# Kernel optimization log

Hardware: AMD Instinct MI355X
Metric: run time of the kernel (lower is better)

Reference implementation:

```python
import jax, jax.numpy as jnp
import numpy as np

B, C, T, H = 256, 8, 1024, 512
WB_INC = 0.05  # task_data_generator.wb_inc


def setup_inputs() -> dict:
    key = jax.random.key(0)
    ks = jax.random.split(key, 8)
    # arms/time strictly positive to keep the likelihood division well-conditioned
    inputs = jax.random.uniform(ks[0], (B, C, T), dtype=jnp.float32) + 0.5
    w_in = jax.random.normal(ks[1], (H, 6), dtype=jnp.float32) / np.sqrt(6.0).astype(np.float32)
    b_in = jax.random.normal(ks[2], (H,), dtype=jnp.float32) * 0.01
    w_rec = jax.random.normal(ks[3], (H, H), dtype=jnp.float32) / np.sqrt(float(H)).astype(np.float32)
    b_rec = jax.random.normal(ks[4], (H,), dtype=jnp.float32) * 0.01
    w_key = jax.random.normal(ks[5], (2, H), dtype=jnp.float32) / np.sqrt(float(H)).astype(np.float32)
    b_key = jax.random.normal(ks[6], (2,), dtype=jnp.float32) * 0.01
    # pre-drawn standard normals for the data-dependent noise injection (one per batch per step)
    z = jax.random.normal(ks[7], (T - 1, B), dtype=jnp.float32)
    return {"inputs": inputs, "w_in": w_in, "b_in": b_in, "w_rec": w_rec,
            "b_rec": b_rec, "w_key": w_key, "b_key": b_key, "z": z}


def _likelihood(tm, arms):
    # ((tm - arm) / (0.15*arm))^2, zeroed where tm == 0
    prs = ((tm[:, None] - arms) / (0.15 * arms)) ** 2
    return jnp.where(tm[:, None] == 0.0, 0.0, prs)


def _forward(inputs, w_in, b_in, w_rec, b_rec, w_key, b_key, z):
    Bsz, _, Tn = inputs.shape
    Hn = w_rec.shape[0]
    in_arms = inputs[:, :6, :]
    tm1 = inputs[:, 6, :]  # (B, T), never modified
    tm2 = inputs[:, 7, :]  # (B, T), receives cumulative noise offsets
    idx_tm1 = jnp.argmax(tm1, axis=1)          # (B,)
    ts = jnp.arange(1, Tn)
    tm1_done = ts[:, None] > idx_tm1[None, :]  # (T-1, B)
    arms_pri = jnp.moveaxis(in_arms[:, :2, 1:], 2, 0)  # (T-1, B, 2)
    arms_sec = jnp.moveaxis(in_arms[:, 2:, 1:], 2, 0)  # (T-1, B, 4)
    tm1_seq = tm1[:, 1:].T                              # (T-1, B)
    tm2_seq = tm2[:, 1:].T                              # (T-1, B)

    def step(carry, xs):
        h_pre, key_h_pre, side_h_pre, offset = carry
        ap, asec, t1, t2o, done, zt = xs
        side_h = key_h_pre > 0.5
        arms_sum = asec[:, :2] * key_h_pre[:, None] + asec[:, 2:] * (1.0 - key_h_pre)[:, None]
        closer1 = jnp.argmin(jnp.abs(ap - t1[:, None]), axis=1) == 0
        away = side_h != closer1
        switched = (side_h != side_h_pre) & done & away
        # in-place suffix update in_time[b,1,t:] += N(0, |wb_inc*tm2_t|) == cumulative per-batch offset
        t2_cur = t2o + offset
        offset = offset + jnp.where(switched, zt * jnp.abs(WB_INC * t2_cur), 0.0)
        t2_eff = t2o + offset
        pr1 = _likelihood(t1, ap)
        pr2 = _likelihood(t2_eff, arms_sum)
        prs_t = jnp.concatenate([pr1, pr2], axis=1)          # (B, 4)
        inp_t = jnp.concatenate([ap, arms_sum, t1[:, None], t2_eff[:, None]], axis=1)  # (B, 6)
        h_t = jnp.tanh(inp_t @ w_in.T + b_in + h_pre @ w_rec.T + b_rec)
        key_t = jax.nn.sigmoid(h_t @ w_key.T + b_key)        # (B, 2)
        return (h_t, key_t[:, 0], side_h, offset), (h_t, prs_t, key_t, t2_eff)

    carry0 = (jnp.zeros((Bsz, Hn), dtype=inputs.dtype),
              jnp.ones((Bsz,), dtype=inputs.dtype),
              jnp.ones((Bsz,), dtype=bool),
              jnp.zeros((Bsz,), dtype=inputs.dtype))
    _, (hs_s, prs_s, keys_s, tm2_s) = jax.lax.scan(
        step, carry0, (arms_pri, arms_sec, tm1_seq, tm2_seq, tm1_done, z))
    # loop starts at t=1; t=0 slots stay zero
    hs = jnp.concatenate([jnp.zeros((Bsz, Hn, 1), dtype=inputs.dtype), jnp.moveaxis(hs_s, 0, 2)], axis=2)
    prs = jnp.concatenate([jnp.zeros((Bsz, 4, 1), dtype=inputs.dtype), jnp.moveaxis(prs_s, 0, 2)], axis=2)
    keys = jnp.concatenate([jnp.zeros((Bsz, 2, 1), dtype=inputs.dtype), jnp.moveaxis(keys_s, 0, 2)], axis=2)
    tm2_mod = jnp.concatenate([tm2[:, :1], tm2_s.T], axis=1)
    tm_modified = jnp.stack([tm1, tm2_mod], axis=1)  # (B, 2, T)
    return keys, prs, hs, tm_modified


def reference(inputs, w_in, b_in, w_rec, b_rec, w_key, b_key, z):
    return _forward(inputs, w_in, b_in, w_rec, b_rec, w_key, b_key, z)
```

## Files before the change

kernel.cpp:

```cpp
#include <hip/hip_runtime.h>
#include <math.h>

#define TN 1024
#define HH 512
#define BB 256
#define NTHR 512
#define NW48 48
#define TSTRIDE 136

#define OFF_KEYS 0L
#define OFF_PRS  524288L
#define OFF_HS   1572864L
#define OFF_TM   135790592L

typedef float f32x4 __attribute__((ext_vector_type(4)));
typedef _Float16 f16x2 __attribute__((ext_vector_type(2)));

__device__ __forceinline__ float sigm(float x) { return 1.0f / (1.0f + expf(-x)); }

__device__ __forceinline__ float dot2(unsigned a, unsigned b, float c) {
#if __has_builtin(__builtin_amdgcn_fdot2)
    return __builtin_amdgcn_fdot2(__builtin_bit_cast(f16x2, a),
                                  __builtin_bit_cast(f16x2, b), c, false);
#else
    const f16x2 x = __builtin_bit_cast(f16x2, a);
    const f16x2 y = __builtin_bit_cast(f16x2, b);
    return fmaf((float)x.y, (float)y.y, fmaf((float)x.x, (float)y.x, c));
#endif
}

__global__ __launch_bounds__(256) void conv_fp16(const float* __restrict__ w,
                                                 _Float16* __restrict__ o) {
    const int i = (blockIdx.x * 256 + threadIdx.x) * 4;
    const f32x4 v = *(const f32x4*)(w + i);
    _Float16 r[4];
    #pragma unroll
    for (int k = 0; k < 4; ++k) r[k] = (_Float16)v[k];
    *(unsigned long long*)(o + i) = *(const unsigned long long*)r;
}

__global__ __launch_bounds__(NTHR, 2)
__attribute__((amdgpu_waves_per_eu(2, 2)))
void rnn_fused(
    const float* __restrict__ in, const float* __restrict__ w_in,
    const float* __restrict__ b_in, const float* __restrict__ b_rec,
    const float* __restrict__ w_key, const float* __restrict__ b_key,
    const float* __restrict__ z, float* __restrict__ out,
    const _Float16* __restrict__ whf)
{
    __shared__ __align__(16) _Float16 wtail[HH][TSTRIDE];
    __shared__ __align__(16) float tbuf[HH][9];
    __shared__ __align__(16) _Float16 hsh[2][HH];
    __shared__ float keysT[2][2][16];
    __shared__ float prsT[2][4][16];
    __shared__ float tmT[2][16];
    __shared__ float inp6[8];
    __shared__ float kred[8][2];

    const int tid = threadIdx.x;
    const int bb  = blockIdx.x;
    const int wv  = tid >> 6, ln = tid & 63;
    const float* inb = in + (long)bb * 8 * TN;
    const unsigned* wrow = (const unsigned*)(whf + (long)tid * HH);

    unsigned wreg[NW48 * 4];
    #pragma unroll
    for (int i = 0; i < NW48; ++i) {
        const uint4 v = *(const uint4*)(wrow + i * 4);
        wreg[i * 4 + 0] = v.x; wreg[i * 4 + 1] = v.y;
        wreg[i * 4 + 2] = v.z; wreg[i * 4 + 3] = v.w;
    }
    #pragma unroll
    for (int i = 0; i < NW48 * 4; ++i) asm volatile("" : "+v"(wreg[i]));

    {
        const uint4* src = (const uint4*)(wrow + 192);
        #pragma unroll
        for (int i = 0; i < 16; ++i) *(uint4*)&wtail[tid][i * 8] = src[i];
    }

    const float bs  = b_in[tid] + b_rec[tid];
    const float wk0 = w_key[tid], wk1 = w_key[HH + tid];
    const float* wip = w_in + tid * 6;
    const float wi0 = wip[0], wi1 = wip[1], wi2 = wip[2];
    const float wi3 = wip[3], wi4 = wip[4], wi5 = wip[5];

    hsh[0][tid] = (_Float16)0.0f;
    tbuf[tid][0] = 0.0f;
    if (tid < 256) {
        f32x4 v = *(const f32x4*)(inb + 6 * TN + tid * 4);
        __builtin_nontemporal_store(v, (f32x4*)(out + OFF_TM + (long)bb * 2 * TN + tid * 4));
    }
    if (tid == 0) {
        keysT[0][0][0] = 0.f; keysT[0][1][0] = 0.f;
        prsT[0][0][0] = 0.f; prsT[0][1][0] = 0.f;
        prsT[0][2][0] = 0.f; prsT[0][3][0] = 0.f;
        tmT[0][0] = inb[7 * TN];
    }
    int idxm = 0;
    if (wv == 0) {
        const float* tp = inb + 6 * TN;
        float bv = -3.0e38f; int bi = 0;
        for (int i = 0; i < 16; ++i) { int tt = i * 64 + ln; float v = tp[tt]; if (v > bv) { bv = v; bi = tt; } }
        #pragma unroll
        for (int m = 1; m < 64; m <<= 1) {
            float ov = __shfl_xor(bv, m); int oi = __shfl_xor(bi, m);
            if (ov > bv || (ov == bv && oi < bi)) { bv = ov; bi = oi; }
        }
        idxm = bi;
    }
    float kh = 1.0f, off = 0.0f; int side_pre = 1;
    float q0=0,q1=0,q2=0,q3=0,q4=0,q5=0,q6=0,q7=0,qz=0;
    const float bk0 = b_key[0], bk1 = b_key[1];
    if (tid == 0) {
        q0=inb[1]; q1=inb[TN+1]; q2=inb[2*TN+1]; q3=inb[3*TN+1];
        q4=inb[4*TN+1]; q5=inb[5*TN+1]; q6=inb[6*TN+1]; q7=inb[7*TN+1];
        qz=z[bb];
    }
    __syncthreads();

    for (int t = 1; t < TN; ++t) {
        const int par1 = (t - 1) & 1, par2 = t & 1;
        const int tile = (t >> 4) & 1, sl = t & 15;

        if (tid == 0) {
            if (t > 1) {
                float k0 = 0.f, k1 = 0.f;
                #pragma unroll
                for (int w = 0; w < 8; ++w) { k0 += kred[w][0]; k1 += kred[w][1]; }
                const float key0 = sigm(k0 + bk0), key1 = sigm(k1 + bk1);
                const int pt = t - 1;
                keysT[(pt >> 4) & 1][0][pt & 15] = key0;
                keysT[(pt >> 4) & 1][1][pt & 15] = key1;
                kh = key0;
            }
            const int side = (kh > 0.5f);
            const float as0 = q2 * kh + q4 * (1.0f - kh);
            const float as1 = q3 * kh + q5 * (1.0f - kh);
            const int closer1 = (fabsf(q0 - q6) <= fabsf(q1 - q6));
            const int done = (t > idxm);
            const int sw = ((side != side_pre) && done && (side != closer1));
            const float t2c = q7 + off;
            if (sw) off += qz * fabsf(0.05f * t2c);
            const float t2e = q7 + off;
            side_pre = side;
            float u0 = (q6 - q0) / (0.15f * q0);    float pr10 = (q6 == 0.f) ? 0.f : u0 * u0;
            float u1 = (q6 - q1) / (0.15f * q1);    float pr11 = (q6 == 0.f) ? 0.f : u1 * u1;
            float u2 = (t2e - as0) / (0.15f * as0); float pr20 = (t2e == 0.f) ? 0.f : u2 * u2;
            float u3 = (t2e - as1) / (0.15f * as1); float pr21 = (t2e == 0.f) ? 0.f : u3 * u3;
            prsT[tile][0][sl] = pr10; prsT[tile][1][sl] = pr11;
            prsT[tile][2][sl] = pr20; prsT[tile][3][sl] = pr21;
            tmT[tile][sl] = t2e;
            inp6[0] = q0; inp6[1] = q1; inp6[2] = as0;
            inp6[3] = as1; inp6[4] = q6; inp6[5] = t2e;
            const int tn = (t < TN - 1) ? t + 1 : t;
            q0 = inb[tn]; q1 = inb[TN + tn]; q2 = inb[2 * TN + tn]; q3 = inb[3 * TN + tn];
            q4 = inb[4 * TN + tn]; q5 = inb[5 * TN + tn]; q6 = inb[6 * TN + tn]; q7 = inb[7 * TN + tn];
            qz = z[(long)(tn - 1) * BB + bb];
        }

        float a0 = 0.f, a1 = 0.f, a2 = 0.f, a3 = 0.f;
        const unsigned* hb = (const unsigned*)&hsh[par1][0];
        #pragma unroll
        for (int i = 0; i < NW48; ++i) {
            const uint4 hu = *(const uint4*)(hb + i * 4);
            a0 = dot2(wreg[i * 4 + 0], hu.x, a0);
            a1 = dot2(wreg[i * 4 + 1], hu.y, a1);
            a2 = dot2(wreg[i * 4 + 2], hu.z, a2);
            a3 = dot2(wreg[i * 4 + 3], hu.w, a3);
        }
        #pragma unroll
        for (int i = 0; i < 16; ++i) {
            const uint4 hu = *(const uint4*)(hb + 192 + i * 4);
            const uint4 wu = *(const uint4*)&wtail[tid][i * 8];
            a0 = dot2(wu.x, hu.x, a0);
            a1 = dot2(wu.y, hu.y, a1);
            a2 = dot2(wu.z, hu.z, a2);
            a3 = dot2(wu.w, hu.w, a3);
        }
        const float sdot = (a0 + a1) + (a2 + a3);
        __syncthreads();

        {
            const float s = sdot + bs
                          + wi0 * inp6[0] + wi1 * inp6[1] + wi2 * inp6[2]
                          + wi3 * inp6[3] + wi4 * inp6[4] + wi5 * inp6[5];
            const float h = tanhf(s);
            hsh[par2][tid] = (_Float16)h;
            tbuf[tid][t & 7] = h;
            float ka0 = h * wk0, ka1 = h * wk1;
            #pragma unroll
            for (int m = 1; m < 64; m <<= 1) { ka0 += __shfl_xor(ka0, m); ka1 += __shfl_xor(ka1, m); }
            if (ln == 0) { kred[wv][0] = ka0; kred[wv][1] = ka1; }
        }
        __syncthreads();

        if ((t & 7) == 7) {
            const int t0 = t - 7;
            const float* tr = &tbuf[tid][0];
            f32x4 v0, v1;
            v0.x = tr[0]; v0.y = tr[1]; v0.z = tr[2]; v0.w = tr[3];
            v1.x = tr[4]; v1.y = tr[5]; v1.z = tr[6]; v1.w = tr[7];
            float* dst = out + OFF_HS + ((long)bb * HH + tid) * TN + t0;
            __builtin_nontemporal_store(v0, (f32x4*)dst);
            __builtin_nontemporal_store(v1, (f32x4*)(dst + 4));
        }
        if ((t & 15) == 0 && wv == 0) {
            const int f = tile ^ 1, t0 = t - 16;
            if (ln < 8) {
                const int ch = ln >> 2, c4 = ln & 3;
                __builtin_nontemporal_store(*(const f32x4*)&keysT[f][ch][c4 * 4],
                    (f32x4*)(out + OFF_KEYS + (long)bb * 2 * TN + ch * TN + t0 + c4 * 4));
            } else if (ln < 24) {
                const int ix = ln - 8, ch = ix >> 2, c4 = ix & 3;
                __builtin_nontemporal_store(*(const f32x4*)&prsT[f][ch][c4 * 4],
                    (f32x4*)(out + OFF_PRS + (long)bb * 4 * TN + ch * TN + t0 + c4 * 4));
            } else if (ln < 28) {
                const int c4 = ln - 24;
                __builtin_nontemporal_store(*(const f32x4*)&tmT[f][c4 * 4],
                    (f32x4*)(out + OFF_TM + (long)bb * 2 * TN + TN + t0 + c4 * 4));
            }
        }
    }

    if (tid == 0) {
        float k0 = 0.f, k1 = 0.f;
        #pragma unroll
        for (int w = 0; w < 8; ++w) { k0 += kred[w][0]; k1 += kred[w][1]; }
        keysT[1][0][15] = sigm(k0 + bk0);
        keysT[1][1][15] = sigm(k1 + bk1);
    }
    __syncthreads();
    if (wv == 0) {
        const int f = 1, t0 = TN - 16;
        if (ln < 8) {
            const int ch = ln >> 2, c4 = ln & 3;
            __builtin_nontemporal_store(*(const f32x4*)&keysT[f][ch][c4 * 4],
                (f32x4*)(out + OFF_KEYS + (long)bb * 2 * TN + ch * TN + t0 + c4 * 4));
        } else if (ln < 24) {
            const int ix = ln - 8, ch = ix >> 2, c4 = ix & 3;
            __builtin_nontemporal_store(*(const f32x4*)&prsT[f][ch][c4 * 4],
                (f32x4*)(out + OFF_PRS + (long)bb * 4 * TN + ch * TN + t0 + c4 * 4));
        } else if (ln < 28) {
            const int c4 = ln - 24;
            __builtin_nontemporal_store(*(const f32x4*)&tmT[f][c4 * 4],
                (f32x4*)(out + OFF_TM + (long)bb * 2 * TN + TN + t0 + c4 * 4));
        }
    }
}

extern "C" void kernel_launch(void* const* d_in, const int* in_sizes, int n_in,
                              void* d_out, int out_size, void* d_ws, size_t ws_size,
                              hipStream_t stream) {
    (void)in_sizes; (void)n_in; (void)out_size; (void)ws_size;
    const float* in    = (const float*)d_in[0];
    const float* w_in  = (const float*)d_in[1];
    const float* b_in  = (const float*)d_in[2];
    const float* w_rec = (const float*)d_in[3];
    const float* b_rec = (const float*)d_in[4];
    const float* w_key = (const float*)d_in[5];
    const float* b_key = (const float*)d_in[6];
    const float* z     = (const float*)d_in[7];
    float* out = (float*)d_out;
    _Float16* whf = (_Float16*)d_ws;

    hipLaunchKernelGGL(conv_fp16, dim3(HH * HH / 1024), dim3(256), 0, stream, w_rec, whf);
    hipLaunchKernelGGL(rnn_fused, dim3(BB), dim3(NTHR), 0, stream,
                       in, w_in, b_in, b_rec, w_key, b_key, z, out, whf);
}
```

Baseline: 3.898 ms.

## Halve register-resident weights and stream middle slice of recurrent weights from global memory

Cuts the per-thread register-cached recurrent weights from 192 to 96 packed fp16 pairs. The next 96 pairs are streamed from global memory (likely L2-resident) on every timestep, and the last 128 stay in shared memory. Thread 0's input prefetch for the next step is replaced by loads for the current step, and the launch-bounds attribute is swapped for an explicit flat-work-group-size. The goal is to relieve register pressure or spills, at the cost of extra global loads inside the serial recurrence loop.

```diff
diff --git a/kernel.cpp b/kernel.cpp
--- a/kernel.cpp
+++ b/kernel.cpp
@@ -5,7 +5,8 @@
 #define HH 512
 #define BB 256
 #define NTHR 512
-#define NW48 48
+#define NWREG 96
+#define NSTRM 24
 #define TSTRIDE 136
 
 #define OFF_KEYS 0L
@@ -39,8 +40,8 @@
     *(unsigned long long*)(o + i) = *(const unsigned long long*)r;
 }
 
-__global__ __launch_bounds__(NTHR, 2)
-__attribute__((amdgpu_waves_per_eu(2, 2)))
+__global__
+__attribute__((amdgpu_flat_work_group_size(512, 512), amdgpu_waves_per_eu(2, 2)))
 void rnn_fused(
     const float* __restrict__ in, const float* __restrict__ w_in,
     const float* __restrict__ b_in, const float* __restrict__ b_rec,
@@ -63,15 +64,15 @@
     const float* inb = in + (long)bb * 8 * TN;
     const unsigned* wrow = (const unsigned*)(whf + (long)tid * HH);
 
-    unsigned wreg[NW48 * 4];
+    unsigned wreg[NWREG];
     #pragma unroll
-    for (int i = 0; i < NW48; ++i) {
+    for (int i = 0; i < NWREG / 4; ++i) {
         const uint4 v = *(const uint4*)(wrow + i * 4);
         wreg[i * 4 + 0] = v.x; wreg[i * 4 + 1] = v.y;
         wreg[i * 4 + 2] = v.z; wreg[i * 4 + 3] = v.w;
     }
     #pragma unroll
-    for (int i = 0; i < NW48 * 4; ++i) asm volatile("" : "+v"(wreg[i]));
+    for (int i = 0; i < NWREG; ++i) asm volatile("" : "+v"(wreg[i]));
 
     {
         const uint4* src = (const uint4*)(wrow + 192);
@@ -110,13 +111,7 @@
         idxm = bi;
     }
     float kh = 1.0f, off = 0.0f; int side_pre = 1;
-    float q0=0,q1=0,q2=0,q3=0,q4=0,q5=0,q6=0,q7=0,qz=0;
     const float bk0 = b_key[0], bk1 = b_key[1];
-    if (tid == 0) {
-        q0=inb[1]; q1=inb[TN+1]; q2=inb[2*TN+1]; q3=inb[3*TN+1];
-        q4=inb[4*TN+1]; q5=inb[5*TN+1]; q6=inb[6*TN+1]; q7=inb[7*TN+1];
-        qz=z[bb];
-    }
     __syncthreads();
 
     for (int t = 1; t < TN; ++t) {
@@ -124,6 +119,11 @@
         const int tile = (t >> 4) & 1, sl = t & 15;
 
         if (tid == 0) {
+            const float q0 = inb[t],          q1 = inb[TN + t];
+            const float q2 = inb[2 * TN + t], q3 = inb[3 * TN + t];
+            const float q4 = inb[4 * TN + t], q5 = inb[5 * TN + t];
+            const float q6 = inb[6 * TN + t], q7 = inb[7 * TN + t];
+            const float qz = z[(long)(t - 1) * BB + bb];
             if (t > 1) {
                 float k0 = 0.f, k1 = 0.f;
                 #pragma unroll
@@ -153,21 +153,26 @@
             tmT[tile][sl] = t2e;
             inp6[0] = q0; inp6[1] = q1; inp6[2] = as0;
             inp6[3] = as1; inp6[4] = q6; inp6[5] = t2e;
-            const int tn = (t < TN - 1) ? t + 1 : t;
-            q0 = inb[tn]; q1 = inb[TN + tn]; q2 = inb[2 * TN + tn]; q3 = inb[3 * TN + tn];
-            q4 = inb[4 * TN + tn]; q5 = inb[5 * TN + tn]; q6 = inb[6 * TN + tn]; q7 = inb[7 * TN + tn];
-            qz = z[(long)(tn - 1) * BB + bb];
         }
 
         float a0 = 0.f, a1 = 0.f, a2 = 0.f, a3 = 0.f;
         const unsigned* hb = (const unsigned*)&hsh[par1][0];
         #pragma unroll
-        for (int i = 0; i < NW48; ++i) {
+        for (int i = 0; i < NWREG / 4; ++i) {
             const uint4 hu = *(const uint4*)(hb + i * 4);
             a0 = dot2(wreg[i * 4 + 0], hu.x, a0);
             a1 = dot2(wreg[i * 4 + 1], hu.y, a1);
             a2 = dot2(wreg[i * 4 + 2], hu.z, a2);
             a3 = dot2(wreg[i * 4 + 3], hu.w, a3);
+        }
+        #pragma unroll
+        for (int i = 0; i < NSTRM; ++i) {
+            const uint4 wu = *(const uint4*)(wrow + NWREG + i * 4);
+            const uint4 hu = *(const uint4*)(hb + NWREG + i * 4);
+            a0 = dot2(wu.x, hu.x, a0);
+            a1 = dot2(wu.y, hu.y, a1);
+            a2 = dot2(wu.z, hu.z, a2);
+            a3 = dot2(wu.w, hu.w, a3);
         }
         #pragma unroll
         for (int i = 0; i < 16; ++i) {
```

New measurement: 3.607 ms. -7.4%, faster.
